# Kernel tuning notes

Measured on AMD Instinct MI355X. Metric: run time of the kernel, lower is better.

The kernel has to match this reference:

```python
import jax, jax.numpy as jnp
import numpy as np

NUM_NODES, NODE_F = 50000, 128
NUM_EDGES, EDGE_F = 500000, 128
B, N = 4096, 100
D = 64      # node_dim
T = 8       # time_dim
LN_EPS = 1e-5


def setup_inputs() -> dict:
    key = jax.random.key(0)
    ks = jax.random.split(key, 16)
    inp = {
        'src_neighbor_node_ids': jax.random.randint(ks[0], (B, N), 0, NUM_NODES),
        'src_neighbor_edge_ids': jax.random.randint(ks[1], (B, N), 0, NUM_EDGES),
        'src_neighbor_times': jax.random.uniform(ks[2], (B, N), dtype=jnp.float32),
        'dst_node_ids': jax.random.randint(ks[3], (B,), 0, NUM_NODES),
        'node_raw_features': jax.random.normal(ks[4], (NUM_NODES, NODE_F), jnp.float32),
        'edge_raw_features': jax.random.normal(ks[5], (NUM_EDGES, EDGE_F), jnp.float32),
        # projection layers (stored as [in, out])
        'W_feat': jax.random.normal(ks[6], (NODE_F, D), jnp.float32) / np.sqrt(NODE_F),
        'b_feat': jnp.zeros((D,), jnp.float32),
        'W_edge': jax.random.normal(ks[7], (1, D), jnp.float32),
        'b_edge': jnp.zeros((D,), jnp.float32),
        'W_time': jax.random.normal(ks[8], (T, D), jnp.float32) / np.sqrt(T),
        'b_time': jnp.zeros((D,), jnp.float32),
        'W_struct': jax.random.normal(ks[9], (1, D), jnp.float32),
        'b_struct': jnp.zeros((D,), jnp.float32),
        # time encoder (cosine basis with log-spaced frequencies)
        'w_tenc': (1.0 / 10 ** np.linspace(0, 9, T)).astype(np.float32),
        'b_tenc': jnp.zeros((T,), jnp.float32),
        # layernorm
        'ln_g': jnp.ones((D,), jnp.float32),
        'ln_b': jnp.zeros((D,), jnp.float32),
        # GCNConv
        'W_gcn': jax.random.normal(ks[10], (D, D), jnp.float32) / np.sqrt(D),
        'b_gcn': jnp.zeros((D,), jnp.float32),
        # output layer
        'W_out': jax.random.normal(ks[11], (D, D), jnp.float32) / np.sqrt(D),
        'b_out': jnp.zeros((D,), jnp.float32),
    }
    return inp


def reference(src_neighbor_node_ids, src_neighbor_edge_ids, src_neighbor_times,
              dst_node_ids, node_raw_features, edge_raw_features,
              W_feat, b_feat, W_edge, b_edge, W_time, b_time, W_struct, b_struct,
              w_tenc, b_tenc, ln_g, ln_b, W_gcn, b_gcn, W_out, b_out):
    f32 = jnp.float32
    nbr_raw = node_raw_features[src_neighbor_node_ids]            # [B,N,F]
    node_f = nbr_raw @ W_feat + b_feat                            # [B,N,D]
    edge_col = edge_raw_features[src_neighbor_edge_ids, 0][..., None]  # [B,N,1]
    edge_f = edge_col @ W_edge + b_edge
    t_enc = jnp.cos(src_neighbor_times[..., None] * w_tenc + b_tenc)   # [B,N,T]
    time_f = t_enc @ W_time + b_time
    co = (src_neighbor_node_ids == dst_node_ids[:, None]).astype(f32)[..., None]
    co_f = co @ W_struct + b_struct
    skill_nbr = nbr_raw[..., 0].astype(jnp.int32)                 # [B,N]
    skill_dst = node_raw_features[dst_node_ids, 0].astype(jnp.int32)  # [B]
    sim = (skill_nbr == skill_dst[:, None]).astype(f32)[..., None]
    sim_f = sim @ W_struct + b_struct
    fused = node_f + edge_f + time_f + co_f + sim_f               # [B,N,D]
    mu = fused.mean(-1, keepdims=True)
    var = ((fused - mu) ** 2).mean(-1, keepdims=True)
    fused = (fused - mu) * jax.lax.rsqrt(var + LN_EPS) * ln_g + ln_b
    # per-sample chain GCN: directed edges j -> j+1 for j in [0, v-2], v = #valid ids,
    # PyG gcn_norm with self loops: deg[j] = 1 + in_degree[j]
    h = fused @ W_gcn                                             # [B,N,D]
    v = (src_neighbor_node_ids > 0).sum(-1)                       # [B]
    pos = jnp.arange(N)[None, :]                                  # [1,N]
    has_in = ((pos >= 1) & (pos < v[:, None])).astype(f32)        # [B,N]
    deg = 1.0 + has_in
    dinv_sqrt = jax.lax.rsqrt(deg)
    h_prev = jnp.pad(h[:, :-1], ((0, 0), (1, 0), (0, 0)))
    d_prev = jnp.pad(dinv_sqrt[:, :-1], ((0, 0), (1, 0)))
    out = h / deg[..., None] + (has_in * d_prev * dinv_sqrt)[..., None] * h_prev + b_gcn
    gnn = jax.nn.relu(out)
    src_emb = gnn.mean(axis=1)                                    # [B,D] global_mean_pool over N
    dst_emb = node_raw_features[dst_node_ids] @ W_feat + b_feat
    src_emb = src_emb @ W_out + b_out
    dst_emb = dst_emb @ W_out + b_out
    return src_emb, dst_emb
```

## Files before the change

### kernel.cpp

```cpp
#include <hip/hip_runtime.h>
#include <stdint.h>

#define NUM_NODES 50000
#define B_ 4096
#define N_ 100

typedef float f32x4 __attribute__((ext_vector_type(4)));
typedef int   i32x4 __attribute__((ext_vector_type(4)));
typedef short s16x8 __attribute__((ext_vector_type(8)));

__device__ inline unsigned short f2bf(float f) {
    unsigned u = __float_as_uint(f);
    u += 0x7fffu + ((u >> 16) & 1u);
    return (unsigned short)(u >> 16);
}

template <int CTRL>
__device__ inline float dpp_add(float x) {
    int t = __builtin_amdgcn_update_dpp(0, __float_as_int(x), CTRL, 0xf, 0xf, true);
    return x + __int_as_float(t);
}
__device__ inline float wave_sum64(float x) {
    x = dpp_add<0x111>(x);
    x = dpp_add<0x112>(x);
    x = dpp_add<0x114>(x);
    x = dpp_add<0x118>(x);
    x = dpp_add<0x142>(x);
    x = dpp_add<0x143>(x);
    return __int_as_float(__builtin_amdgcn_readlane(__float_as_int(x), 63));
}

__global__ __launch_bounds__(256) void k_pre(
    const float* __restrict__ node_raw, const float* __restrict__ W_feat,
    const float* __restrict__ b_feat, const float* __restrict__ W_gcn,
    const float* __restrict__ ln_g, const float* __restrict__ ln_b,
    const float* __restrict__ W_edge, const float* __restrict__ b_edge,
    const float* __restrict__ W_time, const float* __restrict__ b_time,
    const float* __restrict__ W_struct, const float* __restrict__ b_struct,
    float* __restrict__ proj, int* __restrict__ skill,
    float* __restrict__ hb, float* __restrict__ wmg, float* __restrict__ Mg,
    unsigned short* __restrict__ PGmF)
{
    __shared__ float red[4][64];
    __shared__ float PGms[12][64];
    __shared__ unsigned short WfB[16][64][8];
    int blk = blockIdx.x;
    int t = threadIdx.x;
    int dj = t & 63;

    if (blk == gridDim.x - 1) {
        int g = t >> 6;
        float acc = 0.f;
        #pragma unroll
        for (int i = 0; i < 16; ++i) {
            int dk = g * 16 + i;
            acc += ln_b[dk] * W_gcn[dk * 64 + dj];
        }
        red[g][dj] = acc;

        if (t < 64) {
            int d = t;
            float col[11];
            col[0] = W_edge[d];
            col[1] = W_struct[d];
            #pragma unroll
            for (int i = 0; i < 8; ++i) col[2 + i] = W_time[i * 64 + d];
            col[10] = b_edge[d] + b_time[d] + 2.f * b_struct[d];
            float wmv[11];
            #pragma unroll
            for (int j = 0; j < 11; ++j) wmv[j] = wave_sum64(col[j]) * (1.f / 64.f);
            float cc[11];
            #pragma unroll
            for (int j = 0; j < 11; ++j) cc[j] = col[j] - wmv[j];
            #pragma unroll
            for (int j = 0; j < 11; ++j) {
                #pragma unroll
                for (int k = j; k < 11; ++k) {
                    float m = wave_sum64(cc[j] * cc[k]);
                    if (t == 0) { Mg[j * 11 + k] = m; Mg[k * 11 + j] = m; }
                }
            }
            if (t == 0) {
                #pragma unroll
                for (int j = 0; j < 11; ++j) wmg[j] = wmv[j];
            }

            int j = t;
            float accp[12];
            #pragma unroll
            for (int m = 0; m < 12; ++m) accp[m] = 0.f;
            for (int d2 = 0; d2 < 64; ++d2) {
                float gg = ln_g[d2] * W_gcn[d2 * 64 + j];
                float bias_d = b_edge[d2] + b_time[d2] + 2.f * b_struct[d2];
                accp[0] = fmaf(W_edge[d2], gg, accp[0]);
                accp[1] = fmaf(W_struct[d2], gg, accp[1]);
                #pragma unroll
                for (int i = 0; i < 8; ++i)
                    accp[2 + i] = fmaf(W_time[i * 64 + d2], gg, accp[2 + i]);
                accp[10] = fmaf(bias_d, gg, accp[10]);
                accp[11] += gg;
            }
            #pragma unroll
            for (int m = 0; m < 12; ++m) PGms[m][j] = accp[m];
        }
        __syncthreads();
        if (g == 0) hb[dj] = red[0][dj] + red[1][dj] + red[2][dj] + red[3][dj];

        {
            int ct = t >> 6, l = t & 63;
            int col = ct * 16 + (l & 15);
            int ks = (l >> 4) * 8;
            s16x8 a2;
            #pragma unroll
            for (int j2 = 0; j2 < 8; ++j2) {
                int k = ks + j2;
                a2[j2] = (k < 12) ? (short)f2bf(PGms[k][col]) : (short)0;
            }
            *(s16x8*)(PGmF + ((size_t)ct * 64 + l) * 8) = a2;
        }
        return;
    }

    #pragma unroll
    for (int i = 0; i < 4; ++i) {
        int e = t + i * 256;
        int tile = e >> 6;
        int l = e & 63;
        int ct = tile >> 2, kt = tile & 3;
        int col = ct * 16 + (l & 15);
        int ks = kt * 32 + (l >> 4) * 8;
        s16x8 a;
        #pragma unroll
        for (int j = 0; j < 8; ++j)
            a[j] = (short)f2bf(W_feat[(ks + j) * 64 + col]);
        *(s16x8*)&WfB[tile][l][0] = a;
    }
    __syncthreads();

    int w = t >> 6, lane = t & 63;
    int rbase = blk * 64 + w * 16;
    int rA = rbase + (lane & 15);
    int rc = rA < NUM_NODES ? rA : (NUM_NODES - 1);
    int kq = lane >> 4;

    s16x8 A[4];
    float a0x = 0.f;
    #pragma unroll
    for (int kt = 0; kt < 4; ++kt) {
        const float* src = node_raw + (size_t)rc * 128 + kt * 32 + kq * 8;
        f32x4 v0 = *(const f32x4*)src;
        f32x4 v1 = *(const f32x4*)(src + 4);
        s16x8 a;
        a[0] = (short)f2bf(v0.x); a[1] = (short)f2bf(v0.y);
        a[2] = (short)f2bf(v0.z); a[3] = (short)f2bf(v0.w);
        a[4] = (short)f2bf(v1.x); a[5] = (short)f2bf(v1.y);
        a[6] = (short)f2bf(v1.z); a[7] = (short)f2bf(v1.w);
        A[kt] = a;
        if (kt == 0) a0x = v0.x;
    }
    if (kq == 0 && rA < NUM_NODES) skill[rA] = (int)a0x;

    f32x4 acc[4];
    #pragma unroll
    for (int ct = 0; ct < 4; ++ct) { f32x4 z = {0.f,0.f,0.f,0.f}; acc[ct] = z; }
    #pragma unroll
    for (int ct = 0; ct < 4; ++ct) {
        #pragma unroll
        for (int kt = 0; kt < 4; ++kt) {
            s16x8 bfr = *(const s16x8*)&WfB[ct * 4 + kt][lane][0];
            acc[ct] = __builtin_amdgcn_mfma_f32_16x16x32_bf16(A[kt], bfr, acc[ct], 0, 0, 0);
        }
    }
    #pragma unroll
    for (int ct = 0; ct < 4; ++ct) {
        int col = ct * 16 + (lane & 15);
        float bf = b_feat[col];
        #pragma unroll
        for (int j = 0; j < 4; ++j) {
            int row = rbase + kq * 4 + j;
            if (row < NUM_NODES)
                proj[(size_t)row * 64 + col] = acc[ct][j] + bf;
        }
    }
}

__global__ __launch_bounds__(256) void k_pg(
    const float* __restrict__ proj, const float* __restrict__ W_gcn,
    const float* __restrict__ ln_g, float* __restrict__ projG)
{
    __shared__ unsigned short WgB[8][64][8];
    int t = threadIdx.x;
    #pragma unroll
    for (int i = 0; i < 2; ++i) {
        int e = t + i * 256;
        int tile = e >> 6, l = e & 63;
        int ct = tile >> 1, kt = tile & 1;
        int col = ct * 16 + (l & 15);
        int ks = kt * 32 + (l >> 4) * 8;
        s16x8 a;
        #pragma unroll
        for (int j = 0; j < 8; ++j)
            a[j] = (short)f2bf(ln_g[ks + j] * W_gcn[(ks + j) * 64 + col]);
        *(s16x8*)&WgB[tile][l][0] = a;
    }
    __syncthreads();

    int w = t >> 6, lane = t & 63;
    int rbase = blockIdx.x * 64 + w * 16;
    int rA = rbase + (lane & 15);
    int rc = rA < NUM_NODES ? rA : (NUM_NODES - 1);
    int kq = lane >> 4;

    s16x8 Ahi[2], Alo[2];
    #pragma unroll
    for (int kt = 0; kt < 2; ++kt) {
        const float* src = proj + (size_t)rc * 64 + kt * 32 + kq * 8;
        f32x4 v0 = *(const f32x4*)src;
        f32x4 v1 = *(const f32x4*)(src + 4);
        #pragma unroll
        for (int j = 0; j < 8; ++j) {
            float v = (j < 4) ? v0[j] : v1[j - 4];
            unsigned short hi = f2bf(v);
            float rem = v - __uint_as_float((unsigned)hi << 16);
            Ahi[kt][j] = (short)hi;
            Alo[kt][j] = (short)f2bf(rem);
        }
    }
    f32x4 acc[4];
    #pragma unroll
    for (int ct = 0; ct < 4; ++ct) { f32x4 z = {0.f,0.f,0.f,0.f}; acc[ct] = z; }
    #pragma unroll
    for (int ct = 0; ct < 4; ++ct) {
        #pragma unroll
        for (int kt = 0; kt < 2; ++kt) {
            s16x8 bfr = *(const s16x8*)&WgB[ct * 2 + kt][lane][0];
            acc[ct] = __builtin_amdgcn_mfma_f32_16x16x32_bf16(Alo[kt], bfr, acc[ct], 0, 0, 0);
            acc[ct] = __builtin_amdgcn_mfma_f32_16x16x32_bf16(Ahi[kt], bfr, acc[ct], 0, 0, 0);
        }
    }
    #pragma unroll
    for (int ct = 0; ct < 4; ++ct) {
        int col = ct * 16 + (lane & 15);
        #pragma unroll
        for (int j = 0; j < 4; ++j) {
            int row = rbase + kq * 4 + j;
            if (row < NUM_NODES)
                projG[(size_t)row * 64 + col] = acc[ct][j];
        }
    }
}

__global__ __launch_bounds__(256) void k_stat(
    const float* __restrict__ proj,
    const float* __restrict__ W_edge, const float* __restrict__ b_edge,
    const float* __restrict__ W_time, const float* __restrict__ b_time,
    const float* __restrict__ W_struct, const float* __restrict__ b_struct,
    const float* __restrict__ wmg, float* __restrict__ stats)
{
    __shared__ float T[256][65];
    __shared__ float Wc[64][12];
    int t = threadIdx.x;
    int base = blockIdx.x * 256;

    if (t < 64) {
        int d = t;
        Wc[d][0] = W_edge[d];
        Wc[d][1] = W_struct[d];
        #pragma unroll
        for (int i = 0; i < 8; ++i) Wc[d][2 + i] = W_time[i * 64 + d];
        Wc[d][10] = b_edge[d] + b_time[d] + 2.f * b_struct[d];
        Wc[d][11] = 0.f;
    }

    int w = t >> 6, lane = t & 63;
    #pragma unroll 4
    for (int it = 0; it < 64; ++it) {
        int row = it * 4 + w;
        int node = base + row;
        int rc = node < NUM_NODES ? node : (NUM_NODES - 1);
        T[row][lane] = proj[(size_t)rc * 64 + lane];
    }
    __syncthreads();

    float sp = 0.f, spp = 0.f;
    float pw[11];
    #pragma unroll
    for (int j = 0; j < 11; ++j) pw[j] = 0.f;

    for (int d = 0; d < 64; ++d) {
        float p = T[t][d];
        f32x4 c0 = *(const f32x4*)&Wc[d][0];
        f32x4 c1 = *(const f32x4*)&Wc[d][4];
        f32x4 c2 = *(const f32x4*)&Wc[d][8];
        sp += p;
        spp = fmaf(p, p, spp);
        pw[0] = fmaf(p, c0.x, pw[0]);
        pw[1] = fmaf(p, c0.y, pw[1]);
        pw[2] = fmaf(p, c0.z, pw[2]);
        pw[3] = fmaf(p, c0.w, pw[3]);
        pw[4] = fmaf(p, c1.x, pw[4]);
        pw[5] = fmaf(p, c1.y, pw[5]);
        pw[6] = fmaf(p, c1.z, pw[6]);
        pw[7] = fmaf(p, c1.w, pw[7]);
        pw[8] = fmaf(p, c2.x, pw[8]);
        pw[9] = fmaf(p, c2.y, pw[9]);
        pw[10] = fmaf(p, c2.z, pw[10]);
    }

    int node = base + t;
    if (node < NUM_NODES) {
        float o[16];
        o[0] = sp * (1.f / 64.f);
        o[1] = spp - sp * sp * (1.f / 64.f);
        #pragma unroll
        for (int j = 0; j < 11; ++j) o[2 + j] = pw[j] - sp * wmg[j];
        o[13] = 0.f; o[14] = 0.f; o[15] = 0.f;
        float* dst = stats + (size_t)node * 16;
        #pragma unroll
        for (int q = 0; q < 4; ++q) *(f32x4*)(dst + q * 4) = *(f32x4*)&o[q * 4];
    }
}

__global__ __launch_bounds__(256) void k_main(
    const int* __restrict__ ids, const int* __restrict__ eids,
    const float* __restrict__ times, const int* __restrict__ dst_ids,
    const float* __restrict__ edge_raw,
    const float* __restrict__ w_tenc, const float* __restrict__ b_tenc,
    const float* __restrict__ b_gcn, const float* __restrict__ W_out,
    const float* __restrict__ b_out,
    const float* __restrict__ proj, const float* __restrict__ projG,
    const int* __restrict__ skill,
    const float* __restrict__ hb, const float* __restrict__ wmg,
    const float* __restrict__ Mg, const unsigned short* __restrict__ PGmF,
    const float* __restrict__ stats,
    float* __restrict__ out)
{
    __shared__ int ids_s[112];
    __shared__ unsigned short VA[112 * 32];
    __shared__ float rstd_s[112];
    __shared__ float pooled[64];
    __shared__ float x2[64];
    __shared__ int vcnt_w[4];

    int b = blockIdx.x;
    int t = threadIdx.x;
    int lane = t & 63, w = t >> 6;

    int dstb = dst_ids[b];
    int skdst = skill[dstb];

    int idx_c = t < N_ ? t : 0;
    int id_t = ids[b * N_ + idx_c];
    float tm_t = times[b * N_ + idx_c];
    int ei_t = eids[b * N_ + idx_c];
    float e_t = edge_raw[(size_t)ei_t * 128];
    int sk_t = skill[id_t];
    unsigned long long bal = __ballot((t < N_) && (id_t > 0));
    if (lane == 0) vcnt_w[w] = __popcll(bal);

    if (t < N_) {
        ids_s[t] = id_t;
        float u[11];
        u[0] = e_t;
        u[1] = (id_t == dstb ? 1.f : 0.f) + (sk_t == skdst ? 1.f : 0.f);
        #pragma unroll
        for (int i = 0; i < 8; ++i) u[2 + i] = __cosf(fmaf(tm_t, w_tenc[i], b_tenc[i]));
        u[10] = 1.f;

        const f32x4* sp = (const f32x4*)(stats + (size_t)id_t * 16);
        f32x4 s0 = sp[0], s1 = sp[1], s2 = sp[2], s3 = sp[3];
        float pwv[11] = {s0.z, s0.w, s1.x, s1.y, s1.z, s1.w,
                         s2.x, s2.y, s2.z, s2.w, s3.x};
        float mu = s0.x, q = s0.y;
        #pragma unroll
        for (int j = 0; j < 11; ++j) {
            mu = fmaf(u[j], wmg[j], mu);
            q = fmaf(2.f * u[j], pwv[j], q);
        }
        #pragma unroll
        for (int j = 0; j < 11; ++j) {
            float tj = 0.f;
            #pragma unroll
            for (int k = 0; k < 11; ++k) tj = fmaf(Mg[j * 11 + k], u[k], tj);
            q = fmaf(u[j], tj, q);
        }
        float rstd = rsqrtf(fmaxf(q, 0.f) * (1.f / 64.f) + 1e-5f);
        rstd_s[t] = rstd;

        unsigned short vv[32];
        #pragma unroll
        for (int j = 0; j < 11; ++j) vv[j] = f2bf(rstd * u[j]);
        vv[11] = f2bf(-rstd * mu);
        #pragma unroll
        for (int j = 12; j < 32; ++j) vv[j] = 0;
        #pragma unroll
        for (int c = 0; c < 4; ++c)
            *(s16x8*)((char*)VA + t * 64 + ((c ^ (t & 3)) * 16)) = *(const s16x8*)&vv[c * 8];
    } else if (t < 112) {
        ids_s[t] = 0;
        rstd_s[t] = 0.f;
        s16x8 z = {0, 0, 0, 0, 0, 0, 0, 0};
        #pragma unroll
        for (int c = 0; c < 4; ++c)
            *(s16x8*)((char*)VA + t * 64 + c * 16) = z;
    }
    if (w == 2) x2[lane] = proj[(size_t)dstb * 64 + lane];
    __syncthreads();
    int v = vcnt_w[0] + vcnt_w[1] + vcnt_w[2] + vcnt_w[3];

    int colw = 16 * w + (lane & 15);
    int kq = lane >> 4;

    float pgv[7][4];
    #pragma unroll
    for (int mt = 0; mt < 7; ++mt) {
        i32x4 s4 = *(const i32x4*)&ids_s[mt * 16 + kq * 4];
        #pragma unroll
        for (int j = 0; j < 4; ++j)
            pgv[mt][j] = projG[(size_t)s4[j] * 64 + colw];
    }

    s16x8 bfr = *(const s16x8*)(PGmF + ((size_t)w * 64 + lane) * 8);

    f32x4 acc[7];
    #pragma unroll
    for (int mt = 0; mt < 7; ++mt) {
        int row = mt * 16 + (lane & 15);
        s16x8 a = *(const s16x8*)((char*)VA + row * 64 + ((kq ^ (row & 3)) * 16));
        f32x4 z = {0.f, 0.f, 0.f, 0.f};
        acc[mt] = __builtin_amdgcn_mfma_f32_16x16x32_bf16(a, bfr, z, 0, 0, 0);
    }

    float hbv = hb[colw], bgc = b_gcn[colw];
    float carry = 0.f, po = 0.f;
    #pragma unroll
    for (int mt = 0; mt < 7; ++mt) {
        f32x4 rs4 = *(const f32x4*)&rstd_s[mt * 16 + kq * 4];
        float hh[4];
        #pragma unroll
        for (int j = 0; j < 4; ++j)
            hh[j] = fmaf(rs4[j], pgv[mt][j], acc[mt][j]) + hbv;

        float hup = __shfl_up(hh[3], 16, 64);
        float hpj = (kq > 0) ? hup : carry;
        int nb = mt * 16 + kq * 4;
        #pragma unroll
        for (int j = 0; j < 4; ++j) {
            int nn = nb + j;
            bool hin = (nn >= 1) && (nn < v);
            float a_ = hin ? 0.5f : 1.f;
            float dprev = (nn >= 2 && nn <= v) ? 0.70710678118f : 1.f;
            float coef = hin ? dprev * 0.70710678118f : 0.f;
            float o = hh[j] * a_ + coef * hpj + bgc;
            po += (nn < N_) ? fmaxf(o, 0.f) : 0.f;
            hpj = hh[j];
        }
        carry = __shfl(hh[3], 48 + (lane & 15), 64);
    }
    po += __shfl_xor(po, 16, 64);
    po += __shfl_xor(po, 32, 64);
    if (lane < 16) pooled[colw] = po * (1.f / (float)N_);
    __syncthreads();

    if (w == 0) {
        float o = b_out[lane];
        #pragma unroll
        for (int dk4 = 0; dk4 < 16; ++dk4) {
            f32x4 p4 = *(const f32x4*)&pooled[dk4 * 4];
            o = fmaf(p4.x, W_out[(dk4 * 4 + 0) * 64 + lane], o);
            o = fmaf(p4.y, W_out[(dk4 * 4 + 1) * 64 + lane], o);
            o = fmaf(p4.z, W_out[(dk4 * 4 + 2) * 64 + lane], o);
            o = fmaf(p4.w, W_out[(dk4 * 4 + 3) * 64 + lane], o);
        }
        out[(size_t)b * 64 + lane] = o;
    } else if (w == 1) {
        float o = b_out[lane];
        #pragma unroll
        for (int dk4 = 0; dk4 < 16; ++dk4) {
            f32x4 p4 = *(const f32x4*)&x2[dk4 * 4];
            o = fmaf(p4.x, W_out[(dk4 * 4 + 0) * 64 + lane], o);
            o = fmaf(p4.y, W_out[(dk4 * 4 + 1) * 64 + lane], o);
            o = fmaf(p4.z, W_out[(dk4 * 4 + 2) * 64 + lane], o);
            o = fmaf(p4.w, W_out[(dk4 * 4 + 3) * 64 + lane], o);
        }
        out[(size_t)(B_ + b) * 64 + lane] = o;
    }
}

extern "C" void kernel_launch(void* const* d_in, const int* in_sizes, int n_in,
                              void* d_out, int out_size, void* d_ws, size_t ws_size,
                              hipStream_t stream)
{
    const int*   ids      = (const int*)d_in[0];
    const int*   eids     = (const int*)d_in[1];
    const float* times    = (const float*)d_in[2];
    const int*   dst_ids  = (const int*)d_in[3];
    const float* node_raw = (const float*)d_in[4];
    const float* edge_raw = (const float*)d_in[5];
    const float* W_feat   = (const float*)d_in[6];
    const float* b_feat   = (const float*)d_in[7];
    const float* W_edge   = (const float*)d_in[8];
    const float* b_edge   = (const float*)d_in[9];
    const float* W_time   = (const float*)d_in[10];
    const float* b_time   = (const float*)d_in[11];
    const float* W_struct = (const float*)d_in[12];
    const float* b_struct = (const float*)d_in[13];
    const float* w_tenc   = (const float*)d_in[14];
    const float* b_tenc   = (const float*)d_in[15];
    const float* ln_g     = (const float*)d_in[16];
    const float* ln_b     = (const float*)d_in[17];
    const float* W_gcn    = (const float*)d_in[18];
    const float* b_gcn    = (const float*)d_in[19];
    const float* W_out    = (const float*)d_in[20];
    const float* b_out    = (const float*)d_in[21];

    char* ws = (char*)d_ws;
    float*          proj   = (float*)ws;
    int*            skill  = (int*)(ws + 12800000);
    float*          hb     = (float*)(ws + 13008192);
    float*          wmg    = (float*)(ws + 13008448);
    float*          Mg     = (float*)(ws + 13008512);
    unsigned short* PGmF   = (unsigned short*)(ws + 13009024);
    float*          stats  = (float*)(ws + 13100032);
    float*          projG  = (float*)(ws + 16400000);

    k_pre<<<783, 256, 0, stream>>>(node_raw, W_feat, b_feat, W_gcn, ln_g, ln_b,
                                   W_edge, b_edge, W_time, b_time, W_struct, b_struct,
                                   proj, skill, hb, wmg, Mg, PGmF);
    k_stat<<<196, 256, 0, stream>>>(proj, W_edge, b_edge, W_time, b_time,
                                    W_struct, b_struct, wmg, stats);
    k_pg<<<782, 256, 0, stream>>>(proj, W_gcn, ln_g, projG);
    k_main<<<B_, 256, 0, stream>>>(ids, eids, times, dst_ids, edge_raw,
                                   w_tenc, b_tenc, b_gcn, W_out, b_out,
                                   proj, projG, skill, hb, wmg, Mg, PGmF, stats,
                                   (float*)d_out);
}
```

Measured before the change: 74.22 us.

## Fold node stats and dst output projection into MFMA k_pg kernel

Removes the separate k_stat kernel and computes per-node statistics (sums, sum of squares, projections onto edge/time/struct weights) with MFMA inside k_pg, using split hi/lo bf16 operands. k_pg also precomputes the destination-embedding output projection for every node, so k_main only copies a row instead of doing a 64x64 matvec per block. k_main hoists the projG gathers and cosine time encodings before the first barrier and precomputes the GCN coefficients in shared memory. This saves one launch and per-block work, but adds a 12.8MB dstE write for all nodes and moves stats math to a bf16-split MFMA, which may change precision.

```diff
diff --git a/kernel.cpp b/kernel.cpp
--- a/kernel.cpp
+++ b/kernel.cpp
@@ -6,6 +6,7 @@
 #define N_ 100
 
 typedef float f32x4 __attribute__((ext_vector_type(4)));
+typedef float f32x2 __attribute__((ext_vector_type(2)));
 typedef int   i32x4 __attribute__((ext_vector_type(4)));
 typedef short s16x8 __attribute__((ext_vector_type(8)));
 
@@ -186,10 +187,19 @@
 
 __global__ __launch_bounds__(256) void k_pg(
     const float* __restrict__ proj, const float* __restrict__ W_gcn,
-    const float* __restrict__ ln_g, float* __restrict__ projG)
+    const float* __restrict__ ln_g,
+    const float* __restrict__ W_out, const float* __restrict__ b_out,
+    const float* __restrict__ W_edge, const float* __restrict__ b_edge,
+    const float* __restrict__ W_time, const float* __restrict__ b_time,
+    const float* __restrict__ W_struct, const float* __restrict__ b_struct,
+    float* __restrict__ projG, float* __restrict__ dstE,
+    float* __restrict__ stats)
 {
     __shared__ unsigned short WgB[8][64][8];
+    __shared__ unsigned short WoB[8][64][8];
+    __shared__ unsigned short WsB[2][64][8];
     int t = threadIdx.x;
+
     #pragma unroll
     for (int i = 0; i < 2; ++i) {
         int e = t + i * 256;
@@ -197,11 +207,34 @@
         int ct = tile >> 1, kt = tile & 1;
         int col = ct * 16 + (l & 15);
         int ks = kt * 32 + (l >> 4) * 8;
+        s16x8 a, b2;
+        #pragma unroll
+        for (int j = 0; j < 8; ++j) {
+            int k = ks + j;
+            a[j]  = (short)f2bf(ln_g[k] * W_gcn[k * 64 + col]);
+            b2[j] = (short)f2bf(W_out[k * 64 + col]);
+        }
+        *(s16x8*)&WgB[tile][l][0] = a;
+        *(s16x8*)&WoB[tile][l][0] = b2;
+    }
+    if (t < 128) {
+        int kt = t >> 6, l = t & 63;
+        int col = l & 15;
+        int ks = kt * 32 + (l >> 4) * 8;
         s16x8 a;
         #pragma unroll
-        for (int j = 0; j < 8; ++j)
-            a[j] = (short)f2bf(ln_g[ks + j] * W_gcn[(ks + j) * 64 + col]);
-        *(s16x8*)&WgB[tile][l][0] = a;
+        for (int j = 0; j < 8; ++j) {
+            int d = ks + j;
+            float v;
+            if (col == 0) v = W_edge[d];
+            else if (col == 1) v = W_struct[d];
+            else if (col < 10) v = W_time[(col - 2) * 64 + d];
+            else if (col == 10) v = b_edge[d] + b_time[d] + 2.f * b_struct[d];
+            else if (col == 11) v = 1.f;
+            else v = 0.f;
+            a[j] = (short)f2bf(v);
+        }
+        *(s16x8*)&WsB[kt][l][0] = a;
     }
     __syncthreads();
 
@@ -211,7 +244,7 @@
     int rc = rA < NUM_NODES ? rA : (NUM_NODES - 1);
     int kq = lane >> 4;
 
-    s16x8 Ahi[2], Alo[2];
+    s16x8 Ahi[2], Alo[2], Qhi[2], Qlo[2];
     #pragma unroll
     for (int kt = 0; kt < 2; ++kt) {
         const float* src = proj + (size_t)rc * 64 + kt * 32 + kq * 8;
@@ -224,100 +257,69 @@
             float rem = v - __uint_as_float((unsigned)hi << 16);
             Ahi[kt][j] = (short)hi;
             Alo[kt][j] = (short)f2bf(rem);
-        }
-    }
-    f32x4 acc[4];
-    #pragma unroll
-    for (int ct = 0; ct < 4; ++ct) { f32x4 z = {0.f,0.f,0.f,0.f}; acc[ct] = z; }
+            float p2 = v * v;
+            unsigned short h2 = f2bf(p2);
+            float r2 = p2 - __uint_as_float((unsigned)h2 << 16);
+            Qhi[kt][j] = (short)h2;
+            Qlo[kt][j] = (short)f2bf(r2);
+        }
+    }
+
+    f32x4 accG[4], accE[4];
+    f32x4 accS = {0.f, 0.f, 0.f, 0.f}, accQ = {0.f, 0.f, 0.f, 0.f};
     #pragma unroll
     for (int ct = 0; ct < 4; ++ct) {
+        f32x4 z = {0.f, 0.f, 0.f, 0.f};
+        accG[ct] = z; accE[ct] = z;
+    }
+    #pragma unroll
+    for (int ct = 0; ct < 4; ++ct) {
         #pragma unroll
         for (int kt = 0; kt < 2; ++kt) {
-            s16x8 bfr = *(const s16x8*)&WgB[ct * 2 + kt][lane][0];
-            acc[ct] = __builtin_amdgcn_mfma_f32_16x16x32_bf16(Alo[kt], bfr, acc[ct], 0, 0, 0);
-            acc[ct] = __builtin_amdgcn_mfma_f32_16x16x32_bf16(Ahi[kt], bfr, acc[ct], 0, 0, 0);
-        }
-    }
+            s16x8 bg = *(const s16x8*)&WgB[ct * 2 + kt][lane][0];
+            accG[ct] = __builtin_amdgcn_mfma_f32_16x16x32_bf16(Alo[kt], bg, accG[ct], 0, 0, 0);
+            accG[ct] = __builtin_amdgcn_mfma_f32_16x16x32_bf16(Ahi[kt], bg, accG[ct], 0, 0, 0);
+            s16x8 bo = *(const s16x8*)&WoB[ct * 2 + kt][lane][0];
+            accE[ct] = __builtin_amdgcn_mfma_f32_16x16x32_bf16(Alo[kt], bo, accE[ct], 0, 0, 0);
+            accE[ct] = __builtin_amdgcn_mfma_f32_16x16x32_bf16(Ahi[kt], bo, accE[ct], 0, 0, 0);
+        }
+    }
+    #pragma unroll
+    for (int kt = 0; kt < 2; ++kt) {
+        s16x8 bs = *(const s16x8*)&WsB[kt][lane][0];
+        accS = __builtin_amdgcn_mfma_f32_16x16x32_bf16(Alo[kt], bs, accS, 0, 0, 0);
+        accS = __builtin_amdgcn_mfma_f32_16x16x32_bf16(Ahi[kt], bs, accS, 0, 0, 0);
+        accQ = __builtin_amdgcn_mfma_f32_16x16x32_bf16(Qlo[kt], bs, accQ, 0, 0, 0);
+        accQ = __builtin_amdgcn_mfma_f32_16x16x32_bf16(Qhi[kt], bs, accQ, 0, 0, 0);
+    }
+
     #pragma unroll
     for (int ct = 0; ct < 4; ++ct) {
         int col = ct * 16 + (lane & 15);
+        float bo_ = b_out[col];
         #pragma unroll
         for (int j = 0; j < 4; ++j) {
             int row = rbase + kq * 4 + j;
-            if (row < NUM_NODES)
-                projG[(size_t)row * 64 + col] = acc[ct][j];
-        }
-    }
-}
-
-__global__ __launch_bounds__(256) void k_stat(
-    const float* __restrict__ proj,
-    const float* __restrict__ W_edge, const float* __restrict__ b_edge,
-    const float* __restrict__ W_time, const float* __restrict__ b_time,
-    const float* __restrict__ W_struct, const float* __restrict__ b_struct,
-    const float* __restrict__ wmg, float* __restrict__ stats)
-{
-    __shared__ float T[256][65];
-    __shared__ float Wc[64][12];
-    int t = threadIdx.x;
-    int base = blockIdx.x * 256;
-
-    if (t < 64) {
-        int d = t;
-        Wc[d][0] = W_edge[d];
-        Wc[d][1] = W_struct[d];
-        #pragma unroll
-        for (int i = 0; i < 8; ++i) Wc[d][2 + i] = W_time[i * 64 + d];
-        Wc[d][10] = b_edge[d] + b_time[d] + 2.f * b_struct[d];
-        Wc[d][11] = 0.f;
-    }
-
-    int w = t >> 6, lane = t & 63;
-    #pragma unroll 4
-    for (int it = 0; it < 64; ++it) {
-        int row = it * 4 + w;
-        int node = base + row;
-        int rc = node < NUM_NODES ? node : (NUM_NODES - 1);
-        T[row][lane] = proj[(size_t)rc * 64 + lane];
-    }
-    __syncthreads();
-
-    float sp = 0.f, spp = 0.f;
-    float pw[11];
-    #pragma unroll
-    for (int j = 0; j < 11; ++j) pw[j] = 0.f;
-
-    for (int d = 0; d < 64; ++d) {
-        float p = T[t][d];
-        f32x4 c0 = *(const f32x4*)&Wc[d][0];
-        f32x4 c1 = *(const f32x4*)&Wc[d][4];
-        f32x4 c2 = *(const f32x4*)&Wc[d][8];
-        sp += p;
-        spp = fmaf(p, p, spp);
-        pw[0] = fmaf(p, c0.x, pw[0]);
-        pw[1] = fmaf(p, c0.y, pw[1]);
-        pw[2] = fmaf(p, c0.z, pw[2]);
-        pw[3] = fmaf(p, c0.w, pw[3]);
-        pw[4] = fmaf(p, c1.x, pw[4]);
-        pw[5] = fmaf(p, c1.y, pw[5]);
-        pw[6] = fmaf(p, c1.z, pw[6]);
-        pw[7] = fmaf(p, c1.w, pw[7]);
-        pw[8] = fmaf(p, c2.x, pw[8]);
-        pw[9] = fmaf(p, c2.y, pw[9]);
-        pw[10] = fmaf(p, c2.z, pw[10]);
-    }
-
-    int node = base + t;
-    if (node < NUM_NODES) {
-        float o[16];
-        o[0] = sp * (1.f / 64.f);
-        o[1] = spp - sp * sp * (1.f / 64.f);
-        #pragma unroll
-        for (int j = 0; j < 11; ++j) o[2 + j] = pw[j] - sp * wmg[j];
-        o[13] = 0.f; o[14] = 0.f; o[15] = 0.f;
-        float* dst = stats + (size_t)node * 16;
-        #pragma unroll
-        for (int q = 0; q < 4; ++q) *(f32x4*)(dst + q * 4) = *(f32x4*)&o[q * 4];
+            if (row < NUM_NODES) {
+                projG[(size_t)row * 64 + col] = accG[ct][j];
+                dstE[(size_t)row * 64 + col] = accE[ct][j] + bo_;
+            }
+        }
+    }
+    int c = lane & 15;
+    if (c <= 11) {
+        #pragma unroll
+        for (int j = 0; j < 4; ++j) {
+            int row = rbase + kq * 4 + j;
+            if (row < NUM_NODES) stats[(size_t)row * 16 + c] = accS[j];
+        }
+    }
+    if (c == 11) {
+        #pragma unroll
+        for (int j = 0; j < 4; ++j) {
+            int row = rbase + kq * 4 + j;
+            if (row < NUM_NODES) stats[(size_t)row * 16 + 12] = accQ[j];
+        }
     }
 }
 
@@ -328,7 +330,7 @@
     const float* __restrict__ w_tenc, const float* __restrict__ b_tenc,
     const float* __restrict__ b_gcn, const float* __restrict__ W_out,
     const float* __restrict__ b_out,
-    const float* __restrict__ proj, const float* __restrict__ projG,
+    const float* __restrict__ projG, const float* __restrict__ dstE,
     const int* __restrict__ skill,
     const float* __restrict__ hb, const float* __restrict__ wmg,
     const float* __restrict__ Mg, const unsigned short* __restrict__ PGmF,
@@ -338,8 +340,8 @@
     __shared__ int ids_s[112];
     __shared__ unsigned short VA[112 * 32];
     __shared__ float rstd_s[112];
+    __shared__ f32x2 cf_s[112];
     __shared__ float pooled[64];
-    __shared__ float x2[64];
     __shared__ int vcnt_w[4];
 
     int b = blockIdx.x;
@@ -353,30 +355,63 @@
     int id_t = ids[b * N_ + idx_c];
     float tm_t = times[b * N_ + idx_c];
     int ei_t = eids[b * N_ + idx_c];
-    float e_t = edge_raw[(size_t)ei_t * 128];
-    int sk_t = skill[id_t];
+    if (t < 112) ids_s[t] = (t < N_) ? id_t : 0;
     unsigned long long bal = __ballot((t < N_) && (id_t > 0));
     if (lane == 0) vcnt_w[w] = __popcll(bal);
+    float tc[8];
+    #pragma unroll
+    for (int i = 0; i < 8; ++i) tc[i] = __cosf(fmaf(tm_t, w_tenc[i], b_tenc[i]));
+    __syncthreads();
+    int v = vcnt_w[0] + vcnt_w[1] + vcnt_w[2] + vcnt_w[3];
+
+    int colw = 16 * w + (lane & 15);
+    int kq = lane >> 4;
+    float pgv[7][4];
+    #pragma unroll
+    for (int mt = 0; mt < 7; ++mt) {
+        i32x4 s4 = *(const i32x4*)&ids_s[mt * 16 + kq * 4];
+        #pragma unroll
+        for (int j = 0; j < 4; ++j)
+            pgv[mt][j] = projG[(size_t)s4[j] * 64 + colw];
+    }
+    if (w == 3)
+        out[(size_t)(B_ + b) * 64 + lane] = dstE[(size_t)dstb * 64 + lane];
+
+    if (t < 112) {
+        int n = t;
+        bool hin = (n >= 1) && (n < v);
+        float a_ = hin ? 0.5f : 1.f;
+        float dprev = (n >= 2 && n <= v) ? 0.70710678118f : 1.f;
+        float coef = hin ? dprev * 0.70710678118f : 0.f;
+        f32x2 cf = {a_, coef};
+        cf_s[t] = cf;
+    }
 
     if (t < N_) {
-        ids_s[t] = id_t;
+        float e_t = edge_raw[(size_t)ei_t * 128];
+        int sk_t = skill[id_t];
+        const f32x4* sp4 = (const f32x4*)(stats + (size_t)id_t * 16);
+        f32x4 s0 = sp4[0], s1 = sp4[1], s2 = sp4[2];
+        float spp = stats[(size_t)id_t * 16 + 12];
+
         float u[11];
         u[0] = e_t;
         u[1] = (id_t == dstb ? 1.f : 0.f) + (sk_t == skdst ? 1.f : 0.f);
         #pragma unroll
-        for (int i = 0; i < 8; ++i) u[2 + i] = __cosf(fmaf(tm_t, w_tenc[i], b_tenc[i]));
+        for (int i = 0; i < 8; ++i) u[2 + i] = tc[i];
         u[10] = 1.f;
 
-        const f32x4* sp = (const f32x4*)(stats + (size_t)id_t * 16);
-        f32x4 s0 = sp[0], s1 = sp[1], s2 = sp[2], s3 = sp[3];
-        float pwv[11] = {s0.z, s0.w, s1.x, s1.y, s1.z, s1.w,
-                         s2.x, s2.y, s2.z, s2.w, s3.x};
-        float mu = s0.x, q = s0.y;
+        float pwv[11] = {s0.x, s0.y, s0.z, s0.w, s1.x, s1.y, s1.z, s1.w,
+                         s2.x, s2.y, s2.z};
+        float sp = s2.w;
+        float dot_upw = 0.f, su_wm = 0.f;
         #pragma unroll
         for (int j = 0; j < 11; ++j) {
-            mu = fmaf(u[j], wmg[j], mu);
-            q = fmaf(2.f * u[j], pwv[j], q);
-        }
+            dot_upw = fmaf(u[j], pwv[j], dot_upw);
+            su_wm = fmaf(u[j], wmg[j], su_wm);
+        }
+        float mu = sp * (1.f / 64.f) + su_wm;
+        float q = spp + sp * sp * (1.f / 64.f) + 2.f * dot_upw - 2.f * sp * mu;
         #pragma unroll
         for (int j = 0; j < 11; ++j) {
             float tj = 0.f;
@@ -397,31 +432,15 @@
         for (int c = 0; c < 4; ++c)
             *(s16x8*)((char*)VA + t * 64 + ((c ^ (t & 3)) * 16)) = *(const s16x8*)&vv[c * 8];
     } else if (t < 112) {
-        ids_s[t] = 0;
         rstd_s[t] = 0.f;
         s16x8 z = {0, 0, 0, 0, 0, 0, 0, 0};
         #pragma unroll
         for (int c = 0; c < 4; ++c)
             *(s16x8*)((char*)VA + t * 64 + c * 16) = z;
     }
-    if (w == 2) x2[lane] = proj[(size_t)dstb * 64 + lane];
     __syncthreads();
-    int v = vcnt_w[0] + vcnt_w[1] + vcnt_w[2] + vcnt_w[3];
-
-    int colw = 16 * w + (lane & 15);
-    int kq = lane >> 4;
-
-    float pgv[7][4];
-    #pragma unroll
-    for (int mt = 0; mt < 7; ++mt) {
-        i32x4 s4 = *(const i32x4*)&ids_s[mt * 16 + kq * 4];
-        #pragma unroll
-        for (int j = 0; j < 4; ++j)
-            pgv[mt][j] = projG[(size_t)s4[j] * 64 + colw];
-    }
 
     s16x8 bfr = *(const s16x8*)(PGmF + ((size_t)w * 64 + lane) * 8);
-
     f32x4 acc[7];
     #pragma unroll
     for (int mt = 0; mt < 7; ++mt) {
@@ -435,7 +454,10 @@
     float carry = 0.f, po = 0.f;
     #pragma unroll
     for (int mt = 0; mt < 7; ++mt) {
-        f32x4 rs4 = *(const f32x4*)&rstd_s[mt * 16 + kq * 4];
+        int nb = mt * 16 + kq * 4;
+        f32x4 rs4 = *(const f32x4*)&rstd_s[nb];
+        f32x4 cf01 = *(const f32x4*)&cf_s[nb];
+        f32x4 cf23 = *(const f32x4*)&cf_s[nb + 2];
         float hh[4];
         #pragma unroll
         for (int j = 0; j < 4; ++j)
@@ -443,18 +465,16 @@
 
         float hup = __shfl_up(hh[3], 16, 64);
         float hpj = (kq > 0) ? hup : carry;
-        int nb = mt * 16 + kq * 4;
-        #pragma unroll
-        for (int j = 0; j < 4; ++j) {
-            int nn = nb + j;
-            bool hin = (nn >= 1) && (nn < v);
-            float a_ = hin ? 0.5f : 1.f;
-            float dprev = (nn >= 2 && nn <= v) ? 0.70710678118f : 1.f;
-            float coef = hin ? dprev * 0.70710678118f : 0.f;
-            float o = hh[j] * a_ + coef * hpj + bgc;
-            po += (nn < N_) ? fmaxf(o, 0.f) : 0.f;
-            hpj = hh[j];
-        }
+
+        float o0 = fmaf(hh[0], cf01.x, fmaf(cf01.y, hpj, bgc));
+        float o1 = fmaf(hh[1], cf01.z, fmaf(cf01.w, hh[0], bgc));
+        float o2 = fmaf(hh[2], cf23.x, fmaf(cf23.y, hh[1], bgc));
+        float o3 = fmaf(hh[3], cf23.z, fmaf(cf23.w, hh[2], bgc));
+        if (nb < N_)     po += fmaxf(o0, 0.f);
+        if (nb + 1 < N_) po += fmaxf(o1, 0.f);
+        if (nb + 2 < N_) po += fmaxf(o2, 0.f);
+        if (nb + 3 < N_) po += fmaxf(o3, 0.f);
+
         carry = __shfl(hh[3], 48 + (lane & 15), 64);
     }
     po += __shfl_xor(po, 16, 64);
@@ -473,17 +493,6 @@
             o = fmaf(p4.w, W_out[(dk4 * 4 + 3) * 64 + lane], o);
         }
         out[(size_t)b * 64 + lane] = o;
-    } else if (w == 1) {
-        float o = b_out[lane];
-        #pragma unroll
-        for (int dk4 = 0; dk4 < 16; ++dk4) {
-            f32x4 p4 = *(const f32x4*)&x2[dk4 * 4];
-            o = fmaf(p4.x, W_out[(dk4 * 4 + 0) * 64 + lane], o);
-            o = fmaf(p4.y, W_out[(dk4 * 4 + 1) * 64 + lane], o);
-            o = fmaf(p4.z, W_out[(dk4 * 4 + 2) * 64 + lane], o);
-            o = fmaf(p4.w, W_out[(dk4 * 4 + 3) * 64 + lane], o);
-        }
-        out[(size_t)(B_ + b) * 64 + lane] = o;
     }
 }
 
@@ -523,15 +532,16 @@
     unsigned short* PGmF   = (unsigned short*)(ws + 13009024);
     float*          stats  = (float*)(ws + 13100032);
     float*          projG  = (float*)(ws + 16400000);
+    float*          dstE   = (float*)(ws + 29200000);
 
     k_pre<<<783, 256, 0, stream>>>(node_raw, W_feat, b_feat, W_gcn, ln_g, ln_b,
                                    W_edge, b_edge, W_time, b_time, W_struct, b_struct,
                                    proj, skill, hb, wmg, Mg, PGmF);
-    k_stat<<<196, 256, 0, stream>>>(proj, W_edge, b_edge, W_time, b_time,
-                                    W_struct, b_struct, wmg, stats);
-    k_pg<<<782, 256, 0, stream>>>(proj, W_gcn, ln_g, projG);
+    k_pg<<<782, 256, 0, stream>>>(proj, W_gcn, ln_g, W_out, b_out,
+                                  W_edge, b_edge, W_time, b_time, W_struct, b_struct,
+                                  projG, dstE, stats);
     k_main<<<B_, 256, 0, stream>>>(ids, eids, times, dst_ids, edge_raw,
                                    w_tenc, b_tenc, b_gcn, W_out, b_out,
-                                   proj, projG, skill, hb, wmg, Mg, PGmF, stats,
+                                   projG, dstE, skill, hb, wmg, Mg, PGmF, stats,
                                    (float*)d_out);
 }
```

Measured after the change: 70.41 us. 1.05x faster.
